# Kernel tuning notes

Hardware: AMD Instinct MI355X
Metric: run time of the kernel (lower is better)

Reference implementation:

```python
import math
import jax, jax.numpy as jnp
import numpy as np

C = 1.0          # Poincare ball curvature
NUM_HEADS = 8
EPS = 1e-15

def _beta(a, b):
    # Beta function via lgamma (python float constant)
    return math.exp(math.lgamma(a) + math.lgamma(b) - math.lgamma(a + b))

def h_linear(x, z, r, c=C):
    """HNN++ Poincare fully-connected layer (hypll HLinear).
    x: [..., in] points in the ball; z: [in, out] tangent weights; r: [out] bias."""
    sc = math.sqrt(c)
    x2 = jnp.sum(x * x, axis=-1, keepdims=True)
    lam = 2.0 / (1.0 - c * x2)                                # conformal factor
    zn = jnp.maximum(jnp.linalg.norm(z, axis=0), EPS)          # [out]
    inner = x @ z                                              # [..., out]
    two_scr = 2.0 * sc * r
    d = (2.0 * zn / sc) * jnp.arcsinh(
        (sc * inner * lam / zn) * jnp.cosh(two_scr) - (lam - 1.0) * jnp.sinh(two_scr)
    )
    w = jnp.sinh(sc * d) / sc
    return w / (1.0 + jnp.sqrt(1.0 + c * jnp.sum(w * w, axis=-1, keepdims=True)))

def pairwise_dist(q, k, c=C):
    """Poincare distance d(q,k) = arccosh(1 + 2c|q-k|^2 / ((1-c|q|^2)(1-c|k|^2))) / sqrt(c).
    q,k: [B,H,S,hd] -> [B,H,S,S]."""
    q2 = jnp.sum(q * q, axis=-1)
    k2 = jnp.sum(k * k, axis=-1)
    qk = jnp.einsum('bhqd,bhkd->bhqk', q, k)
    diff2 = jnp.maximum(q2[..., :, None] + k2[..., None, :] - 2.0 * qk, 0.0)
    denom = (1.0 - c * q2)[..., :, None] * (1.0 - c * k2)[..., None, :]
    arg = 1.0 + 2.0 * c * diff2 / denom
    return jnp.arccosh(jnp.maximum(arg, 1.0 + 1e-7)) / math.sqrt(c)

def midpoint(v, w, c=C):
    """Weighted Mobius gyromidpoint: m = 1/2 (x) (sum w*lam*x / sum w*(lam-1)).
    v: [B,H,Sk,hd], w: [B,H,Sq,Sk] -> [B,H,Sq,hd]."""
    v2 = jnp.sum(v * v, axis=-1)                      # [B,H,Sk]
    lam = 2.0 / (1.0 - c * v2)
    num = jnp.einsum('bhqk,bhkd->bhqd', w * lam[..., None, :], v)
    den = jnp.maximum(jnp.einsum('bhqk,bhk->bhq', w, lam - 1.0), EPS)[..., None]
    g = num / den                                     # gyromidpoint pre-scaling
    sc = math.sqrt(c)
    gn = jnp.maximum(jnp.linalg.norm(g, axis=-1, keepdims=True), EPS)
    t = jnp.tanh(0.5 * jnp.arctanh(jnp.clip(sc * gn, 0.0, 1.0 - 1e-7)))
    return (t / sc) * g / gn

def _forward(query, key, value, Wq, bq, Wk, bk, Wv, bv, scale_tau, scale_gamma):
    B, S, E = query.shape
    H = NUM_HEADS
    hd = E // H
    # hyperbolic q/k/v projections, then split into heads: [B,H,S,hd]
    q = h_linear(query, Wq, bq).reshape(B, S, H, hd).transpose(0, 2, 1, 3)
    k = h_linear(key, Wk, bk).reshape(B, S, H, hd).transpose(0, 2, 1, 3)
    v = h_linear(value, Wv, bv).reshape(B, S, H, hd).transpose(0, 2, 1, 3)
    # similarity = -dist/tau - gamma with tau = exp(-scale_tau)
    sim = -pairwise_dist(q, k) * jnp.exp(scale_tau[0]) - scale_gamma[0]
    causal = jnp.triu(jnp.ones((S, S), dtype=bool), k=1)
    sim = jnp.where(causal, -jnp.inf, sim)
    w = jnp.exp(sim)                                  # 'exp' attention activation
    agg = midpoint(v, w)                              # [B,H,S,hd]
    agg = agg.transpose(0, 2, 1, 3).reshape(B, S, E)
    # HNN++ beta-concatenation of the per-head ball points
    scale = _beta(E / 2.0, 0.5) / _beta(hd / 2.0, 0.5)
    return agg * scale

def setup_inputs() -> dict:
    root = jax.random.key(0)
    ks = jax.random.split(root, 8)
    B, S, E = 1, 2048, 512
    s = 0.02  # keep points well inside the unit ball
    return {
        'query': s * jax.random.normal(ks[0], (B, S, E), jnp.float32),
        'key':   s * jax.random.normal(ks[1], (B, S, E), jnp.float32),
        'value': s * jax.random.normal(ks[2], (B, S, E), jnp.float32),
        'Wq': s * jax.random.normal(ks[3], (E, E), jnp.float32),
        'Wk': s * jax.random.normal(ks[4], (E, E), jnp.float32),
        'Wv': s * jax.random.normal(ks[5], (E, E), jnp.float32),
        'bq': jnp.zeros((E,), jnp.float32),
        'bk': jnp.zeros((E,), jnp.float32),
        'bv': jnp.zeros((E,), jnp.float32),
        'scale_tau': jnp.zeros((1,), jnp.float32),
        'scale_gamma': jnp.zeros((1,), jnp.float32),
    }

def reference(query, key, value, Wq, Wk, Wv, bq, bk, bv, scale_tau, scale_gamma):
    return _forward(query, key, value, Wq, bq, Wk, bk, Wv, bv, scale_tau, scale_gamma)
```

## Files before the change

### kernel.cpp

```cpp
#include <hip/hip_runtime.h>
#include <cmath>

#define H 8
#define SEQ 2048
#define EDIM 512
#define HD 64
#define EPSF 1e-15f

typedef short bf16x8 __attribute__((ext_vector_type(8)));
typedef float f32x4 __attribute__((ext_vector_type(4)));

#define ZN_OFF    16
#define ACC_OFF   (ZN_OFF + 3 * EDIM)
#define STATS_OFF (ACC_OFF + H * SEQ * 80)
#define CQ_OFF    (STATS_OFF + 3 * H * SEQ)
#define IK_OFF    (CQ_OFF + H * SEQ)
#define U16_OFF   (IK_OFF + H * SEQ + 16)
#define WT_U16    0
#define QKVB_U16  (WT_U16 + 3 * EDIM * EDIM)
#define VT_U16    (QKVB_U16 + 3 * SEQ * EDIM)

__device__ __forceinline__ float bf2f(unsigned short u){
  union { unsigned int i; float f; } v; v.i = ((unsigned int)u) << 16; return v.f;
}
__device__ __forceinline__ unsigned short f2bf(float f){
  union { float f; unsigned int i; } v; v.f = f;
  unsigned int x = v.i;
  unsigned int r = (x + 0x7fffu + ((x >> 16) & 1u)) >> 16;
  return (unsigned short)r;
}

__device__ __forceinline__ int detect_f32(const unsigned short* __restrict__ q){
  const int l = threadIdx.x & 63;
  float mx = 0.f;
  #pragma unroll
  for (int j = 0; j < 4; ++j) mx = fmaxf(mx, fabsf(bf2f(q[l * 4 + j])));
  #pragma unroll
  for (int m = 32; m >= 1; m >>= 1) mx = fmaxf(mx, __shfl_xor(mx, m, 64));
  return mx > 1000.f;
}

__global__ __launch_bounds__(256) void wcvt_kernel(
    const void* __restrict__ Wq, const void* __restrict__ Wk, const void* __restrict__ Wv,
    const unsigned short* __restrict__ qprobe,
    unsigned short* __restrict__ WT, float* __restrict__ zn)
{
  const int p = blockIdx.y;
  const int bi = blockIdx.x >> 3, bo = blockIdx.x & 7;
  const void* W = (p == 0) ? Wq : ((p == 1) ? Wk : Wv);
  const int t = threadIdx.x;
  const int isf32 = detect_f32(qprobe);
  __shared__ float tile[64][65];

  #pragma unroll
  for (int j = 0; j < 16; ++j){
    int idx = t + 256 * j;
    int il = idx >> 6, ol = idx & 63;
    float val;
    if (isf32) val = ((const float*)W)[(size_t)(bi * 64 + il) * EDIM + bo * 64 + ol];
    else       val = bf2f(((const unsigned short*)W)[(size_t)(bi * 64 + il) * EDIM + bo * 64 + ol]);
    tile[il][ol] = val;
  }
  __syncthreads();
  if (t < 64){
    float s = 0.f;
    #pragma unroll 8
    for (int i = 0; i < 64; ++i){ float v = tile[i][t]; s += v * v; }
    atomicAdd(&zn[p * EDIM + bo * 64 + t], s);
  }
  #pragma unroll
  for (int j = 0; j < 16; ++j){
    int idx = t + 256 * j;
    int ol = idx >> 6, il = idx & 63;
    WT[((size_t)p * EDIM + bo * 64 + ol) * EDIM + bi * 64 + il] = f2bf(tile[il][ol]);
  }
}

__global__ __launch_bounds__(256) void hlinear_kernel(
    const void* __restrict__ Xq, const void* __restrict__ Xk, const void* __restrict__ Xv,
    const unsigned short* __restrict__ WT,
    const void* __restrict__ Bq, const void* __restrict__ Bk, const void* __restrict__ Bv,
    const float* __restrict__ znacc,
    unsigned short* __restrict__ qkvb, float* __restrict__ stats,
    float* __restrict__ cqs, float* __restrict__ iks,
    unsigned short* __restrict__ VT)
{
  const int p = blockIdx.y;
  const void* X  = (p == 0) ? Xq : ((p == 1) ? Xk : Xv);
  const void* Bb = (p == 0) ? Bq : ((p == 1) ? Bk : Bv);
  const int r0 = blockIdx.x * 16;
  const int t  = threadIdx.x;
  const int w = t >> 6, lane = t & 63;
  const int col = lane & 15, quad = lane >> 4;
  const int isf32 = detect_f32((const unsigned short*)Xq);

  __shared__ float smem[16 * EDIM];
  __shared__ float sw2[16];

  const unsigned short* WTb = WT + ((size_t)p * EDIM + w * 128 + col) * EDIM;
  const float* Xf = (const float*)X + (size_t)(r0 + col) * EDIM;
  const unsigned short* Xh = (const unsigned short*)X + (size_t)(r0 + col) * EDIM;

  f32x4 acc[8];
  #pragma unroll
  for (int nt = 0; nt < 8; ++nt) acc[nt] = (f32x4){0.f, 0.f, 0.f, 0.f};
  float x2part = 0.f;

  for (int ks = 0; ks < 16; ++ks){
    bf16x8 af;
    if (isf32){
      float4 xa = *(const float4*)&Xf[ks * 32 + quad * 8];
      float4 xb = *(const float4*)&Xf[ks * 32 + quad * 8 + 4];
      float xv[8] = {xa.x, xa.y, xa.z, xa.w, xb.x, xb.y, xb.z, xb.w};
      #pragma unroll
      for (int j = 0; j < 8; ++j){ af[j] = (short)f2bf(xv[j]); x2part += xv[j] * xv[j]; }
    } else {
      af = *(const bf16x8*)&Xh[ks * 32 + quad * 8];
      #pragma unroll
      for (int j = 0; j < 8; ++j){ float xv = bf2f((unsigned short)af[j]); x2part += xv * xv; }
    }
    #pragma unroll
    for (int nt = 0; nt < 8; ++nt){
      bf16x8 bf = *(const bf16x8*)&WTb[(size_t)nt * 16 * EDIM + ks * 32 + quad * 8];
      acc[nt] = __builtin_amdgcn_mfma_f32_16x16x32_bf16(af, bf, acc[nt], 0, 0, 0);
    }
  }
  x2part += __shfl_xor(x2part, 16, 64);
  x2part += __shfl_xor(x2part, 32, 64);
  float lamr[4], lm1[4];
  #pragma unroll
  for (int r = 0; r < 4; ++r){
    float x2r = __shfl(x2part, quad * 4 + r, 64);
    lamr[r] = 2.f / (1.f - x2r);
    lm1[r] = lamr[r] - 1.f;
  }
  #pragma unroll
  for (int nt = 0; nt < 8; ++nt){
    const int n = w * 128 + nt * 16 + col;
    float znv = fmaxf(sqrtf(znacc[p * EDIM + n]), EPSF);
    float rb;
    if (isf32) rb = ((const float*)Bb)[n];
    else       rb = bf2f(((const unsigned short*)Bb)[n]);
    float e2r = __expf(2.f * rb);
    float ie2r = 1.f / e2r;
    float ch = 0.5f * (e2r + ie2r), sh = 0.5f * (e2r - ie2r);
    float izn = 1.f / znv;
    float tz = 2.f * znv;
    #pragma unroll
    for (int r = 0; r < 4; ++r){
      float a = (acc[nt][r] * lamr[r] * izn) * ch - lm1[r] * sh;
      float b = a + sqrtf(a * a + 1.f);
      float tt = __expf(tz * __logf(b));
      smem[(quad * 4 + r) * EDIM + n] = 0.5f * (tt - 1.f / tt);
    }
  }
  __syncthreads();

  {
    int row = t >> 4, l = t & 15;
    float s = 0.f;
    for (int o = l; o < EDIM; o += 16){ float wv = smem[row * EDIM + o]; s += wv * wv; }
    #pragma unroll
    for (int m = 8; m >= 1; m >>= 1) s += __shfl_xor(s, m, 16);
    if (l == 0) sw2[row] = s;
  }
  __syncthreads();

  const int o0 = 2 * t;
  const int h0 = t >> 5;
  const int d0 = o0 & 63;
  const int l5 = t & 31;
  #pragma unroll
  for (int rr = 0; rr < 16; ++rr){
    float inv = 1.f / (1.f + sqrtf(1.f + sw2[rr]));
    unsigned short b0 = f2bf(smem[rr * EDIM + o0] * inv);
    unsigned short b1 = f2bf(smem[rr * EDIM + o0 + 1] * inv);
    float r0v = bf2f(b0), r1v = bf2f(b1);
    int s = r0 + rr;
    unsigned int* dst = (unsigned int*)&qkvb[(((size_t)p * H + h0) * SEQ + s) * HD + d0];
    *dst = (unsigned int)b0 | ((unsigned int)b1 << 16);
    float ss = r0v * r0v + r1v * r1v;
    #pragma unroll
    for (int m = 16; m >= 1; m >>= 1) ss += __shfl_xor(ss, m, 64);
    if (p == 2){
      float lam = 2.f / (1.f - ss);
      VT[((size_t)h0 * 80 + d0) * SEQ + s]     = f2bf(r0v * lam);
      VT[((size_t)h0 * 80 + d0 + 1) * SEQ + s] = f2bf(r1v * lam);
      if (l5 < 16)
        VT[((size_t)h0 * 80 + 64 + l5) * SEQ + s] = (l5 == 0) ? f2bf(lam - 1.f) : 0;
    }
    if (l5 == 0){
      stats[((size_t)p * H + h0) * SEQ + s] = ss;
      if (p == 0) cqs[(size_t)h0 * SEQ + s] = 2.f / (1.f - ss);
      if (p == 1) iks[(size_t)h0 * SEQ + s] = 1.f / (1.f - ss);
    }
  }
}

__global__ __launch_bounds__(256) void attn_kernel(
    const unsigned short* __restrict__ Qb, const unsigned short* __restrict__ Kb,
    const unsigned short* __restrict__ VT,
    const float* __restrict__ q2s_all, const float* __restrict__ k2s_all,
    const float* __restrict__ cqs_all, const float* __restrict__ iks_all,
    const void* __restrict__ tau, const void* __restrict__ gam,
    const unsigned short* __restrict__ qprobe,
    float* __restrict__ ACC)
{
  const int h  = blockIdx.y;
  const int tile = blockIdx.x >> 3;
  const int sl = blockIdx.x & 7;
  if (sl > tile) return;
  const int t = threadIdx.x;
  const int w = t >> 6, lane = t & 63;
  const int col = lane & 15, quad = lane >> 4;
  const int q0 = tile * 64 + w * 16;

  const unsigned short* Qh  = Qb + (size_t)h * SEQ * HD;
  const unsigned short* Kh  = Kb + (size_t)h * SEQ * HD;
  const unsigned short* VTh = VT + (size_t)h * 80 * SEQ;
  const float* q2s = q2s_all + (size_t)h * SEQ;
  const float* k2s = k2s_all + (size_t)h * SEQ;
  const float* cqs = cqs_all + (size_t)h * SEQ;
  const float* iks = iks_all + (size_t)h * SEQ;

  const int isf32 = detect_f32(qprobe);
  float tauv, gamv;
  if (isf32){ tauv = ((const float*)tau)[0]; gamv = ((const float*)gam)[0]; }
  else      { tauv = bf2f(((const unsigned short*)tau)[0]);
              gamv = bf2f(((const unsigned short*)gam)[0]); }
  const float e_tau = __expf(tauv);

  const int srcA = ((quad & 1) * 2) * 16 + col;
  const int srcB = srcA + 16;
  const int tsel = quad >> 1;

  bf16x8 qf0 = *(const bf16x8*)&Qh[(size_t)(q0 + col) * HD + quad * 8];
  bf16x8 qf1 = *(const bf16x8*)&Qh[(size_t)(q0 + col) * HD + 32 + quad * 8];
  const float q2 = q2s[q0 + col];
  const float cq = cqs[q0 + col];
  const int qmax = q0 + col;

  f32x4 pv[5];
  #pragma unroll
  for (int nt = 0; nt < 5; ++nt) pv[nt] = (f32x4){0.f, 0.f, 0.f, 0.f};

  #pragma unroll 2
  for (int kc = sl; kc <= tile; kc += 8){
    #pragma unroll
    for (int half = 0; half < 2; ++half){
      const int kb32 = kc * 64 + half * 32;
      unsigned int tlo[2], thi[2];
      #pragma unroll
      for (int tt = 0; tt < 2; ++tt){
        const int kbase = kb32 + 16 * tt;
        bf16x8 kf0 = *(const bf16x8*)&Kh[(size_t)(kbase + col) * HD + quad * 8];
        bf16x8 kf1 = *(const bf16x8*)&Kh[(size_t)(kbase + col) * HD + 32 + quad * 8];
        f32x4 s = (f32x4){0.f, 0.f, 0.f, 0.f};
        s = __builtin_amdgcn_mfma_f32_16x16x32_bf16(kf0, qf0, s, 0, 0, 0);
        s = __builtin_amdgcn_mfma_f32_16x16x32_bf16(kf1, qf1, s, 0, 0, 0);
        float4 k2q = *(const float4*)&k2s[kbase + quad * 4];
        float4 ikq = *(const float4*)&iks[kbase + quad * 4];
        unsigned short pb[4];
        #pragma unroll
        for (int r = 0; r < 4; ++r){
          float k2 = (r == 0) ? k2q.x : (r == 1) ? k2q.y : (r == 2) ? k2q.z : k2q.w;
          float ik = (r == 0) ? ikq.x : (r == 1) ? ikq.y : (r == 2) ? ikq.z : ikq.w;
          float diff2 = fmaxf(q2 + k2 - 2.f * s[r], 0.f);
          float u = fmaxf(diff2 * cq * ik, 1e-7f);
          float z = 1.f + u + sqrtf(u * (u + 2.f));
          float dist = __logf(z);
          float wv = __expf(-e_tau * dist - gamv);
          int key = kbase + quad * 4 + r;
          if (key > qmax) wv = 0.f;
          pb[r] = f2bf(wv);
        }
        tlo[tt] = (unsigned int)pb[0] | ((unsigned int)pb[1] << 16);
        thi[tt] = (unsigned int)pb[2] | ((unsigned int)pb[3] << 16);
      }
      unsigned int a0 = (unsigned int)__shfl((int)tlo[0], srcA, 64);
      unsigned int a1 = (unsigned int)__shfl((int)tlo[1], srcA, 64);
      unsigned int b0 = (unsigned int)__shfl((int)thi[0], srcA, 64);
      unsigned int b1 = (unsigned int)__shfl((int)thi[1], srcA, 64);
      unsigned int c0 = (unsigned int)__shfl((int)tlo[0], srcB, 64);
      unsigned int c1 = (unsigned int)__shfl((int)tlo[1], srcB, 64);
      unsigned int d0 = (unsigned int)__shfl((int)thi[0], srcB, 64);
      unsigned int d1 = (unsigned int)__shfl((int)thi[1], srcB, 64);
      union { uint4 u; bf16x8 v; } pw;
      pw.u.x = tsel ? a1 : a0;
      pw.u.y = tsel ? b1 : b0;
      pw.u.z = tsel ? c1 : c0;
      pw.u.w = tsel ? d1 : d0;
      #pragma unroll
      for (int nt = 0; nt < 5; ++nt){
        bf16x8 vf = *(const bf16x8*)&VTh[(size_t)(16 * nt + col) * SEQ + kb32 + quad * 8];
        pv[nt] = __builtin_amdgcn_mfma_f32_16x16x32_bf16(pw.v, vf, pv[nt], 0, 0, 0);
      }
    }
  }

  #pragma unroll
  for (int r = 0; r < 4; ++r){
    float* row = ACC + ((size_t)h * SEQ + q0 + quad * 4 + r) * 80;
    #pragma unroll
    for (int nt = 0; nt < 5; ++nt)
      atomicAdd(&row[16 * nt + col], pv[nt][r]);
  }
}

__global__ __launch_bounds__(64) void attn_fin_kernel(
    const float* __restrict__ ACC, float* __restrict__ out, float beta_scale)
{
  const int h = blockIdx.y, tile = blockIdx.x;
  const int t = threadIdx.x;
  const int col = t & 15, quad = t >> 4;
  const int q0 = tile * 16;

  f32x4 pv[5];
  #pragma unroll
  for (int nt = 0; nt < 5; ++nt)
    #pragma unroll
    for (int r = 0; r < 4; ++r)
      pv[nt][r] = ACC[((size_t)h * SEQ + q0 + quad * 4 + r) * 80 + 16 * nt + col];

  #pragma unroll
  for (int r = 0; r < 4; ++r){
    float den = __shfl(pv[4][r], quad * 16, 64);
    den = fmaxf(den, EPSF);
    float inv_den = 1.f / den;
    float g[4];
    float gsq = 0.f;
    #pragma unroll
    for (int nt = 0; nt < 4; ++nt){ g[nt] = pv[nt][r] * inv_den; gsq += g[nt] * g[nt]; }
    #pragma unroll
    for (int m = 8; m >= 1; m >>= 1) gsq += __shfl_xor(gsq, m, 64);
    float gn = fmaxf(sqrtf(gsq), EPSF);
    float x = fminf(gn, 1.f - 1e-7f);
    float tt2 = x / (1.f + sqrtf(1.f - x * x));
    float scl = (tt2 / gn) * beta_scale;
    const int q = q0 + quad * 4 + r;
    #pragma unroll
    for (int nt = 0; nt < 4; ++nt)
      out[(size_t)q * EDIM + h * HD + 16 * nt + col] = g[nt] * scl;
  }
}

extern "C" void kernel_launch(void* const* d_in, const int* in_sizes, int n_in,
                              void* d_out, int out_size, void* d_ws, size_t ws_size,
                              hipStream_t stream){
  const void* Xq  = d_in[0];
  const void* Xk  = d_in[1];
  const void* Xv  = d_in[2];
  const void* Wq  = d_in[3];
  const void* Wk  = d_in[4];
  const void* Wv  = d_in[5];
  const void* Bq  = d_in[6];
  const void* Bk  = d_in[7];
  const void* Bv  = d_in[8];
  const void* tau = d_in[9];
  const void* gam = d_in[10];

  float* wsf   = (float*)d_ws;
  float* zn    = wsf + ZN_OFF;
  float* ACC   = wsf + ACC_OFF;
  float* stats = wsf + STATS_OFF;
  float* cqs   = wsf + CQ_OFF;
  float* iks   = wsf + IK_OFF;
  unsigned short* u16b = (unsigned short*)(wsf + U16_OFF);
  unsigned short* WT   = u16b + WT_U16;
  unsigned short* qkvb = u16b + QKVB_U16;
  unsigned short* VT   = u16b + VT_U16;

  unsigned short* Qb = qkvb;
  unsigned short* Kb = qkvb + (size_t)H * SEQ * HD;
  float* q2s = stats;
  float* k2s = stats + (size_t)H * SEQ;
  const unsigned short* qprobe = (const unsigned short*)Xq;

  double lb1 = lgamma(EDIM / 2.0) + lgamma(0.5) - lgamma(EDIM / 2.0 + 0.5);
  double lb2 = lgamma(HD / 2.0)   + lgamma(0.5) - lgamma(HD / 2.0 + 0.5);
  float beta_scale = (float)exp(lb1 - lb2);

  hipMemsetAsync(zn, 0, (size_t)(3 * EDIM + H * SEQ * 80) * sizeof(float), stream);
  wcvt_kernel<<<dim3(64, 3), dim3(256), 0, stream>>>(Wq, Wk, Wv, qprobe, WT, zn);
  hlinear_kernel<<<dim3(SEQ / 16, 3), dim3(256), 0, stream>>>(
      Xq, Xk, Xv, WT, Bq, Bk, Bv, zn, qkvb, stats, cqs, iks, VT);
  attn_kernel<<<dim3(32 * 8, H), dim3(256), 0, stream>>>(
      Qb, Kb, VT, q2s, k2s, cqs, iks, tau, gam, qprobe, ACC);
  attn_fin_kernel<<<dim3(128, H), dim3(64), 0, stream>>>(
      ACC, (float*)d_out, beta_scale);
}
```

Before: 217.9 us.

## Halve hlinear row tile and software-prefetch K fragments in attention loop

The hlinear kernel now handles 8 rows per block instead of 16, which doubles the grid and halves shared memory per block. The MFMA A operand duplicates rows, so half of the lanes' results go unused. The attention kernel's key loop becomes a flat loop over half-chunks that loads the next K fragments and k2/ik stats into registers while the current chunk is computed, hiding global-load latency. The cost is more register pressure and wasted MFMA work in hlinear.

```diff
diff --git a/kernel.cpp b/kernel.cpp
--- a/kernel.cpp
+++ b/kernel.cpp
@@ -88,18 +88,18 @@
   const int p = blockIdx.y;
   const void* X  = (p == 0) ? Xq : ((p == 1) ? Xk : Xv);
   const void* Bb = (p == 0) ? Bq : ((p == 1) ? Bk : Bv);
-  const int r0 = blockIdx.x * 16;
+  const int r0 = blockIdx.x * 8;
   const int t  = threadIdx.x;
   const int w = t >> 6, lane = t & 63;
   const int col = lane & 15, quad = lane >> 4;
   const int isf32 = detect_f32((const unsigned short*)Xq);
 
-  __shared__ float smem[16 * EDIM];
-  __shared__ float sw2[16];
+  __shared__ float smem[8 * EDIM];
+  __shared__ float sw2[8];
 
   const unsigned short* WTb = WT + ((size_t)p * EDIM + w * 128 + col) * EDIM;
-  const float* Xf = (const float*)X + (size_t)(r0 + col) * EDIM;
-  const unsigned short* Xh = (const unsigned short*)X + (size_t)(r0 + col) * EDIM;
+  const float* Xf = (const float*)X + (size_t)(r0 + (col & 7)) * EDIM;
+  const unsigned short* Xh = (const unsigned short*)X + (size_t)(r0 + (col & 7)) * EDIM;
 
   f32x4 acc[8];
   #pragma unroll
@@ -127,41 +127,44 @@
   }
   x2part += __shfl_xor(x2part, 16, 64);
   x2part += __shfl_xor(x2part, 32, 64);
-  float lamr[4], lm1[4];
-  #pragma unroll
-  for (int r = 0; r < 4; ++r){
-    float x2r = __shfl(x2part, quad * 4 + r, 64);
-    lamr[r] = 2.f / (1.f - x2r);
-    lm1[r] = lamr[r] - 1.f;
-  }
-  #pragma unroll
-  for (int nt = 0; nt < 8; ++nt){
-    const int n = w * 128 + nt * 16 + col;
-    float znv = fmaxf(sqrtf(znacc[p * EDIM + n]), EPSF);
-    float rb;
-    if (isf32) rb = ((const float*)Bb)[n];
-    else       rb = bf2f(((const unsigned short*)Bb)[n]);
-    float e2r = __expf(2.f * rb);
-    float ie2r = 1.f / e2r;
-    float ch = 0.5f * (e2r + ie2r), sh = 0.5f * (e2r - ie2r);
-    float izn = 1.f / znv;
-    float tz = 2.f * znv;
+
+  if (quad < 2){
+    float lamr[4], lm1[4];
     #pragma unroll
     for (int r = 0; r < 4; ++r){
-      float a = (acc[nt][r] * lamr[r] * izn) * ch - lm1[r] * sh;
-      float b = a + sqrtf(a * a + 1.f);
-      float tt = __expf(tz * __logf(b));
-      smem[(quad * 4 + r) * EDIM + n] = 0.5f * (tt - 1.f / tt);
+      float x2r = __shfl(x2part, quad * 4 + r, 64);
+      lamr[r] = 2.f / (1.f - x2r);
+      lm1[r] = lamr[r] - 1.f;
+    }
+    #pragma unroll
+    for (int nt = 0; nt < 8; ++nt){
+      const int n = w * 128 + nt * 16 + col;
+      float znv = fmaxf(sqrtf(znacc[p * EDIM + n]), EPSF);
+      float rb;
+      if (isf32) rb = ((const float*)Bb)[n];
+      else       rb = bf2f(((const unsigned short*)Bb)[n]);
+      float e2r = __expf(2.f * rb);
+      float ie2r = 1.f / e2r;
+      float ch = 0.5f * (e2r + ie2r), sh = 0.5f * (e2r - ie2r);
+      float izn = 1.f / znv;
+      float tz = 2.f * znv;
+      #pragma unroll
+      for (int r = 0; r < 4; ++r){
+        float a = (acc[nt][r] * lamr[r] * izn) * ch - lm1[r] * sh;
+        float b = a + sqrtf(a * a + 1.f);
+        float tt = __expf(tz * __logf(b));
+        smem[(quad * 4 + r) * EDIM + n] = 0.5f * (tt - 1.f / tt);
+      }
     }
   }
   __syncthreads();
 
   {
-    int row = t >> 4, l = t & 15;
+    int row = t >> 5, l = t & 31;
     float s = 0.f;
-    for (int o = l; o < EDIM; o += 16){ float wv = smem[row * EDIM + o]; s += wv * wv; }
-    #pragma unroll
-    for (int m = 8; m >= 1; m >>= 1) s += __shfl_xor(s, m, 16);
+    for (int o = l; o < EDIM; o += 32){ float wv = smem[row * EDIM + o]; s += wv * wv; }
+    #pragma unroll
+    for (int m = 16; m >= 1; m >>= 1) s += __shfl_xor(s, m, 64);
     if (l == 0) sw2[row] = s;
   }
   __syncthreads();
@@ -171,7 +174,7 @@
   const int d0 = o0 & 63;
   const int l5 = t & 31;
   #pragma unroll
-  for (int rr = 0; rr < 16; ++rr){
+  for (int rr = 0; rr < 8; ++rr){
     float inv = 1.f / (1.f + sqrtf(1.f + sw2[rr]));
     unsigned short b0 = f2bf(smem[rr * EDIM + o0] * inv);
     unsigned short b1 = f2bf(smem[rr * EDIM + o0 + 1] * inv);
@@ -244,58 +247,86 @@
   #pragma unroll
   for (int nt = 0; nt < 5; ++nt) pv[nt] = (f32x4){0.f, 0.f, 0.f, 0.f};
 
-  #pragma unroll 2
-  for (int kc = sl; kc <= tile; kc += 8){
-    #pragma unroll
-    for (int half = 0; half < 2; ++half){
-      const int kb32 = kc * 64 + half * 32;
-      unsigned int tlo[2], thi[2];
+  const int nch = ((tile - sl) >> 3) + 1;
+  const int nhalf = nch * 2;
+  int kb32 = sl * 64;
+
+  bf16x8 ckf0[2], ckf1[2], nkf0[2], nkf1[2];
+  float4 ck2[2], cik[2], nk2[2], nik[2];
+  #pragma unroll
+  for (int tt = 0; tt < 2; ++tt){
+    const int kbase = kb32 + 16 * tt;
+    ckf0[tt] = *(const bf16x8*)&Kh[(size_t)(kbase + col) * HD + quad * 8];
+    ckf1[tt] = *(const bf16x8*)&Kh[(size_t)(kbase + col) * HD + 32 + quad * 8];
+    ck2[tt]  = *(const float4*)&k2s[kbase + quad * 4];
+    cik[tt]  = *(const float4*)&iks[kbase + quad * 4];
+  }
+
+  for (int i = 0; i < nhalf; ++i){
+    const int nkb32 = (i & 1) ? (kb32 + 512 - 32) : (kb32 + 32);
+    const bool have_next = (i + 1 < nhalf);
+    if (have_next){
       #pragma unroll
       for (int tt = 0; tt < 2; ++tt){
-        const int kbase = kb32 + 16 * tt;
-        bf16x8 kf0 = *(const bf16x8*)&Kh[(size_t)(kbase + col) * HD + quad * 8];
-        bf16x8 kf1 = *(const bf16x8*)&Kh[(size_t)(kbase + col) * HD + 32 + quad * 8];
-        f32x4 s = (f32x4){0.f, 0.f, 0.f, 0.f};
-        s = __builtin_amdgcn_mfma_f32_16x16x32_bf16(kf0, qf0, s, 0, 0, 0);
-        s = __builtin_amdgcn_mfma_f32_16x16x32_bf16(kf1, qf1, s, 0, 0, 0);
-        float4 k2q = *(const float4*)&k2s[kbase + quad * 4];
-        float4 ikq = *(const float4*)&iks[kbase + quad * 4];
-        unsigned short pb[4];
-        #pragma unroll
-        for (int r = 0; r < 4; ++r){
-          float k2 = (r == 0) ? k2q.x : (r == 1) ? k2q.y : (r == 2) ? k2q.z : k2q.w;
-          float ik = (r == 0) ? ikq.x : (r == 1) ? ikq.y : (r == 2) ? ikq.z : ikq.w;
-          float diff2 = fmaxf(q2 + k2 - 2.f * s[r], 0.f);
-          float u = fmaxf(diff2 * cq * ik, 1e-7f);
-          float z = 1.f + u + sqrtf(u * (u + 2.f));
-          float dist = __logf(z);
-          float wv = __expf(-e_tau * dist - gamv);
-          int key = kbase + quad * 4 + r;
-          if (key > qmax) wv = 0.f;
-          pb[r] = f2bf(wv);
-        }
-        tlo[tt] = (unsigned int)pb[0] | ((unsigned int)pb[1] << 16);
-        thi[tt] = (unsigned int)pb[2] | ((unsigned int)pb[3] << 16);
+        const int kbase = nkb32 + 16 * tt;
+        nkf0[tt] = *(const bf16x8*)&Kh[(size_t)(kbase + col) * HD + quad * 8];
+        nkf1[tt] = *(const bf16x8*)&Kh[(size_t)(kbase + col) * HD + 32 + quad * 8];
+        nk2[tt]  = *(const float4*)&k2s[kbase + quad * 4];
+        nik[tt]  = *(const float4*)&iks[kbase + quad * 4];
       }
-      unsigned int a0 = (unsigned int)__shfl((int)tlo[0], srcA, 64);
-      unsigned int a1 = (unsigned int)__shfl((int)tlo[1], srcA, 64);
-      unsigned int b0 = (unsigned int)__shfl((int)thi[0], srcA, 64);
-      unsigned int b1 = (unsigned int)__shfl((int)thi[1], srcA, 64);
-      unsigned int c0 = (unsigned int)__shfl((int)tlo[0], srcB, 64);
-      unsigned int c1 = (unsigned int)__shfl((int)tlo[1], srcB, 64);
-      unsigned int d0 = (unsigned int)__shfl((int)thi[0], srcB, 64);
-      unsigned int d1 = (unsigned int)__shfl((int)thi[1], srcB, 64);
-      union { uint4 u; bf16x8 v; } pw;
-      pw.u.x = tsel ? a1 : a0;
-      pw.u.y = tsel ? b1 : b0;
-      pw.u.z = tsel ? c1 : c0;
-      pw.u.w = tsel ? d1 : d0;
-      #pragma unroll
-      for (int nt = 0; nt < 5; ++nt){
-        bf16x8 vf = *(const bf16x8*)&VTh[(size_t)(16 * nt + col) * SEQ + kb32 + quad * 8];
-        pv[nt] = __builtin_amdgcn_mfma_f32_16x16x32_bf16(pw.v, vf, pv[nt], 0, 0, 0);
+    }
+
+    unsigned int tlo[2], thi[2];
+    #pragma unroll
+    for (int tt = 0; tt < 2; ++tt){
+      const int kbase = kb32 + 16 * tt;
+      f32x4 s = (f32x4){0.f, 0.f, 0.f, 0.f};
+      s = __builtin_amdgcn_mfma_f32_16x16x32_bf16(ckf0[tt], qf0, s, 0, 0, 0);
+      s = __builtin_amdgcn_mfma_f32_16x16x32_bf16(ckf1[tt], qf1, s, 0, 0, 0);
+      unsigned short pb[4];
+      #pragma unroll
+      for (int r = 0; r < 4; ++r){
+        float k2 = (r == 0) ? ck2[tt].x : (r == 1) ? ck2[tt].y : (r == 2) ? ck2[tt].z : ck2[tt].w;
+        float ik = (r == 0) ? cik[tt].x : (r == 1) ? cik[tt].y : (r == 2) ? cik[tt].z : cik[tt].w;
+        float diff2 = fmaxf(q2 + k2 - 2.f * s[r], 0.f);
+        float u = fmaxf(diff2 * cq * ik, 1e-7f);
+        float z = 1.f + u + sqrtf(u * (u + 2.f));
+        float dist = __logf(z);
+        float wv = __expf(-e_tau * dist - gamv);
+        int key = kbase + quad * 4 + r;
+        if (key > qmax) wv = 0.f;
+        pb[r] = f2bf(wv);
       }
-    }
+      tlo[tt] = (unsigned int)pb[0] | ((unsigned int)pb[1] << 16);
+      thi[tt] = (unsigned int)pb[2] | ((unsigned int)pb[3] << 16);
+    }
+    unsigned int a0 = (unsigned int)__shfl((int)tlo[0], srcA, 64);
+    unsigned int a1 = (unsigned int)__shfl((int)tlo[1], srcA, 64);
+    unsigned int b0 = (unsigned int)__shfl((int)thi[0], srcA, 64);
+    unsigned int b1 = (unsigned int)__shfl((int)thi[1], srcA, 64);
+    unsigned int c0 = (unsigned int)__shfl((int)tlo[0], srcB, 64);
+    unsigned int c1 = (unsigned int)__shfl((int)tlo[1], srcB, 64);
+    unsigned int d0 = (unsigned int)__shfl((int)thi[0], srcB, 64);
+    unsigned int d1 = (unsigned int)__shfl((int)thi[1], srcB, 64);
+    union { uint4 u; bf16x8 v; } pw;
+    pw.u.x = tsel ? a1 : a0;
+    pw.u.y = tsel ? b1 : b0;
+    pw.u.z = tsel ? c1 : c0;
+    pw.u.w = tsel ? d1 : d0;
+    #pragma unroll
+    for (int nt = 0; nt < 5; ++nt){
+      bf16x8 vf = *(const bf16x8*)&VTh[(size_t)(16 * nt + col) * SEQ + kb32 + quad * 8];
+      pv[nt] = __builtin_amdgcn_mfma_f32_16x16x32_bf16(pw.v, vf, pv[nt], 0, 0, 0);
+    }
+
+    if (have_next){
+      #pragma unroll
+      for (int tt = 0; tt < 2; ++tt){
+        ckf0[tt] = nkf0[tt]; ckf1[tt] = nkf1[tt];
+        ck2[tt] = nk2[tt];   cik[tt] = nik[tt];
+      }
+    }
+    kb32 = nkb32;
   }
 
   #pragma unroll
@@ -382,7 +413,7 @@
 
   hipMemsetAsync(zn, 0, (size_t)(3 * EDIM + H * SEQ * 80) * sizeof(float), stream);
   wcvt_kernel<<<dim3(64, 3), dim3(256), 0, stream>>>(Wq, Wk, Wv, qprobe, WT, zn);
-  hlinear_kernel<<<dim3(SEQ / 16, 3), dim3(256), 0, stream>>>(
+  hlinear_kernel<<<dim3(SEQ / 8, 3), dim3(256), 0, stream>>>(
       Xq, Xk, Xv, WT, Bq, Bk, Bv, zn, qkvb, stats, cqs, iks, VT);
   attn_kernel<<<dim3(32 * 8, H), dim3(256), 0, stream>>>(
       Qb, Kb, VT, q2s, k2s, cqs, iks, tau, gam, qprobe, ACC);
```

Measured after the change: 233.1 us. +7.0%, slower.
